# Performance work log

Measured on AMD Instinct MI355X. Metric: run time of the kernel, lower is better.

The kernel has to match this reference:

```python
import jax, jax.numpy as jnp
import numpy as np

H_DIM = 1024
GATE_DIM = 128


def setup_inputs() -> dict:
    key = jax.random.key(0)
    ks = jax.random.split(key, 7)
    B, L = 32, 2048
    bound_g = 1.0 / np.sqrt(GATE_DIM)
    bound_l = 1.0 / np.sqrt(GATE_DIM)
    return {
        "x": jax.random.normal(ks[0], (B, L, H_DIM), dtype=jnp.float32),
        # GRUCell params (PyTorch layout: rows ordered [r; z; n])
        "weight_ih": jax.random.uniform(ks[1], (3 * GATE_DIM, H_DIM), minval=-bound_g, maxval=bound_g, dtype=jnp.float32),
        "weight_hh": jax.random.uniform(ks[2], (3 * GATE_DIM, GATE_DIM), minval=-bound_g, maxval=bound_g, dtype=jnp.float32),
        "bias_ih": jax.random.uniform(ks[3], (3 * GATE_DIM,), minval=-bound_g, maxval=bound_g, dtype=jnp.float32),
        "bias_hh": jax.random.uniform(ks[4], (3 * GATE_DIM,), minval=-bound_g, maxval=bound_g, dtype=jnp.float32),
        # output linear (gate_dim -> 1)
        "lin_w": jax.random.uniform(ks[5], (1, GATE_DIM), minval=-bound_l, maxval=bound_l, dtype=jnp.float32),
        "lin_b": jax.random.uniform(ks[6], (1,), minval=-bound_l, maxval=bound_l, dtype=jnp.float32),
    }


def reference(x, weight_ih, weight_hh, bias_ih, bias_hh, lin_w, lin_b):
    """Faithful to the original PingHead.forward: `s` is never updated, so every
    timestep runs the GRUCell against a ZERO hidden state. weight_hh @ h == 0,
    leaving only bias_hh contributions. This lets us vectorize over (B, L)."""
    G = GATE_DIM
    # input projection for all gates: (B, L, 3G)
    gi = jnp.einsum('blh,gh->blg', x, weight_ih) + bias_ih
    i_r, i_z, i_n = gi[..., :G], gi[..., G:2 * G], gi[..., 2 * G:]
    b_hr, b_hz, b_hn = bias_hh[:G], bias_hh[G:2 * G], bias_hh[2 * G:]
    r = jax.nn.sigmoid(i_r + b_hr)
    z = jax.nn.sigmoid(i_z + b_hz)
    n = jnp.tanh(i_n + r * b_hn)
    h = (1.0 - z) * n  # + z * 0 (hidden state is always zero)
    # linear(gate_dim -> 1), squeeze last dim -> (B, L)
    out = jnp.einsum('blg,og->blo', h, lin_w) + lin_b
    return out[..., 0]
```

## Files before the change

### kernel.cpp

```cpp
#include <hip/hip_runtime.h>

#define H_DIM   1024
#define G_DIM   128
#define N_DIM   384
#define M_TOTAL 65536
#define BM      64
#define LDA     72

typedef _Float16 half8  __attribute__((ext_vector_type(8)));
typedef float    f32x4  __attribute__((ext_vector_type(4)));

__device__ __forceinline__ float sigmoidf_(float v) {
    return 1.0f / (1.0f + __expf(-v));
}

__global__ __launch_bounds__(256) void prep_w_kernel(const float* __restrict__ w,
                                                     _Float16* __restrict__ wf) {
    int gid  = blockIdx.x * 256 + threadIdx.x;
    int lane = gid & 63;
    int fid  = gid >> 6;
    int ktg  = fid & 31;
    int ct   = fid >> 5;
    int col  = ct * 16 + (lane & 15);
    int kb   = ktg * 32 + (lane >> 4) * 8;
    const f32x4* src = (const f32x4*)(w + (size_t)col * H_DIM + kb);
    f32x4 v0 = src[0], v1 = src[1];
    half8 h;
    #pragma unroll
    for (int j = 0; j < 4; ++j) { h[j] = (_Float16)v0[j]; h[4 + j] = (_Float16)v1[j]; }
    *(half8*)(wf + (size_t)gid * 8) = h;
}

__global__ __launch_bounds__(256) void ping_main_kernel(
    const float* __restrict__ x, const _Float16* __restrict__ wf,
    const float* __restrict__ bias_ih, const float* __restrict__ bias_hh,
    const float* __restrict__ lin_w, const float* __restrict__ lin_b,
    float* __restrict__ out)
{
    __shared__ _Float16 shA[BM * LDA];
    __shared__ float sh_out[BM];

    const int t    = threadIdx.x;
    const int lane = t & 63;
    const int wv   = t >> 6;
    const int ln   = lane & 15;
    const int quad = lane >> 4;

    if (t < BM) sh_out[t] = 0.0f;

    const size_t row0 = (size_t)blockIdx.x * BM;

    f32x4 acc[6][4];
    #pragma unroll
    for (int i = 0; i < 6; ++i)
        #pragma unroll
        for (int rt = 0; rt < 4; ++rt)
            acc[i][rt] = (f32x4){0.f, 0.f, 0.f, 0.f};

    const int rs = t >> 2;
    const int kg = (t & 3) * 16;
    const float* xrow = x + (row0 + rs) * (size_t)H_DIM + kg;
    _Float16* sA = &shA[rs * LDA + kg];

    const half8* bbase = (const half8*)wf;

    for (int kb = 0; kb < H_DIM / 64; ++kb) {
        __syncthreads();
        const f32x4* src = (const f32x4*)(xrow + kb * 64);
        f32x4 v0 = src[0], v1 = src[1], v2 = src[2], v3 = src[3];
        half8 h0, h1;
        #pragma unroll
        for (int j = 0; j < 4; ++j) {
            h0[j] = (_Float16)v0[j]; h0[4 + j] = (_Float16)v1[j];
            h1[j] = (_Float16)v2[j]; h1[4 + j] = (_Float16)v3[j];
        }
        *(half8*)sA       = h0;
        *(half8*)(sA + 8) = h1;
        __syncthreads();

        #pragma unroll
        for (int kt = 0; kt < 2; ++kt) {
            const int ktg = kb * 2 + kt;
            half8 a[4];
            #pragma unroll
            for (int rt = 0; rt < 4; ++rt)
                a[rt] = *(const half8*)&shA[(rt * 16 + ln) * LDA + kt * 32 + quad * 8];
            half8 b[6];
            #pragma unroll
            for (int i = 0; i < 6; ++i) {
                const int ct = ((i >> 1) * 8) + 2 * wv + (i & 1);
                b[i] = bbase[(size_t)(ct * 32 + ktg) * 64 + lane];
            }
            #pragma unroll
            for (int i = 0; i < 6; ++i)
                #pragma unroll
                for (int rt = 0; rt < 4; ++rt)
                    acc[i][rt] = __builtin_amdgcn_mfma_f32_16x16x32_f16(a[rt], b[i], acc[i][rt], 0, 0, 0);
        }
    }

    float psum[4][4];
    #pragma unroll
    for (int rt = 0; rt < 4; ++rt)
        #pragma unroll
        for (int reg = 0; reg < 4; ++reg)
            psum[rt][reg] = 0.f;

    #pragma unroll
    for (int i = 0; i < 2; ++i) {
        const int g = 32 * wv + 16 * i + ln;
        const float b_ir = bias_ih[g];
        const float b_iz = bias_ih[G_DIM + g];
        const float b_in = bias_ih[2 * G_DIM + g];
        const float b_hr = bias_hh[g];
        const float b_hz = bias_hh[G_DIM + g];
        const float b_hn = bias_hh[2 * G_DIM + g];
        const float lw   = lin_w[g];
        #pragma unroll
        for (int rt = 0; rt < 4; ++rt) {
            #pragma unroll
            for (int reg = 0; reg < 4; ++reg) {
                const float r = sigmoidf_(acc[i][rt][reg] + b_ir + b_hr);
                const float z = sigmoidf_(acc[2 + i][rt][reg] + b_iz + b_hz);
                const float n = tanhf(acc[4 + i][rt][reg] + b_in + r * b_hn);
                psum[rt][reg] += lw * (1.0f - z) * n;
            }
        }
    }

    #pragma unroll
    for (int rt = 0; rt < 4; ++rt)
        #pragma unroll
        for (int reg = 0; reg < 4; ++reg) {
            const int row = rt * 16 + quad * 4 + reg;
            atomicAdd(&sh_out[row], psum[rt][reg]);
        }

    __syncthreads();
    if (t < BM) out[row0 + t] = sh_out[t] + lin_b[0];
}

extern "C" void kernel_launch(void* const* d_in, const int* in_sizes, int n_in,
                              void* d_out, int out_size, void* d_ws, size_t ws_size,
                              hipStream_t stream) {
    const float* x      = (const float*)d_in[0];
    const float* w_ih   = (const float*)d_in[1];
    const float* b_ih   = (const float*)d_in[3];
    const float* b_hh   = (const float*)d_in[4];
    const float* lin_w  = (const float*)d_in[5];
    const float* lin_b  = (const float*)d_in[6];
    float* out          = (float*)d_out;
    _Float16* wf        = (_Float16*)d_ws;

    hipLaunchKernelGGL(prep_w_kernel, dim3((N_DIM / 16) * 32 * 64 / 256), dim3(256), 0, stream,
                       w_ih, wf);
    hipLaunchKernelGGL(ping_main_kernel, dim3(M_TOTAL / BM), dim3(256), 0, stream,
                       x, wf, b_ih, b_hh, lin_w, lin_b, out);
}
```

Measured before the change: 434.8 us.

## Double-buffer A tile in LDS with register prefetch, fast tanh and shuffle reduction

Adds a two-buffer LDS ring for the x tile. The next K-block's global loads are issued into registers before the MFMA work on the current block, so load latency is hidden and only one barrier per iteration remains. It also uses packed RTZ fp16 conversion, replaces tanhf with an exp-based formula, and reduces partial sums across lanes with xor shuffles before the LDS atomics. The costs are higher register and LDS use, plus slightly different rounding from round-toward-zero conversion.

```diff
diff --git a/kernel.cpp b/kernel.cpp
--- a/kernel.cpp
+++ b/kernel.cpp
@@ -6,12 +6,30 @@
 #define M_TOTAL 65536
 #define BM      64
 #define LDA     72
+#define ABUF    (BM * LDA)
 
 typedef _Float16 half8  __attribute__((ext_vector_type(8)));
+typedef __fp16   fp16x2 __attribute__((ext_vector_type(2)));
 typedef float    f32x4  __attribute__((ext_vector_type(4)));
 
-__device__ __forceinline__ float sigmoidf_(float v) {
+__device__ __forceinline__ float fast_sigmoid(float v) {
     return 1.0f / (1.0f + __expf(-v));
+}
+__device__ __forceinline__ float fast_tanh(float v) {
+    return 1.0f - 2.0f / (__expf(2.0f * v) + 1.0f);
+}
+
+__device__ __forceinline__ half8 cvt8(f32x4 a, f32x4 b) {
+    fp16x2 p0 = __builtin_amdgcn_cvt_pkrtz(a[0], a[1]);
+    fp16x2 p1 = __builtin_amdgcn_cvt_pkrtz(a[2], a[3]);
+    fp16x2 p2 = __builtin_amdgcn_cvt_pkrtz(b[0], b[1]);
+    fp16x2 p3 = __builtin_amdgcn_cvt_pkrtz(b[2], b[3]);
+    half8 h;
+    h[0] = (_Float16)p0[0]; h[1] = (_Float16)p0[1];
+    h[2] = (_Float16)p1[0]; h[3] = (_Float16)p1[1];
+    h[4] = (_Float16)p2[0]; h[5] = (_Float16)p2[1];
+    h[6] = (_Float16)p3[0]; h[7] = (_Float16)p3[1];
+    return h;
 }
 
 __global__ __launch_bounds__(256) void prep_w_kernel(const float* __restrict__ w,
@@ -37,7 +55,7 @@
     const float* __restrict__ lin_w, const float* __restrict__ lin_b,
     float* __restrict__ out)
 {
-    __shared__ _Float16 shA[BM * LDA];
+    __shared__ _Float16 shA[2 * ABUF];
     __shared__ float sh_out[BM];
 
     const int t    = threadIdx.x;
@@ -59,44 +77,54 @@
 
     const int rs = t >> 2;
     const int kg = (t & 3) * 16;
-    const float* xrow = x + (row0 + rs) * (size_t)H_DIM + kg;
-    _Float16* sA = &shA[rs * LDA + kg];
+    const float* xptr = x + (row0 + rs) * (size_t)H_DIM + kg;
+    _Float16* sW0 = &shA[rs * LDA + kg];
+    _Float16* sW1 = sW0 + ABUF;
 
-    const half8* bbase = (const half8*)wf;
+    const _Float16* pb[6];
+    #pragma unroll
+    for (int i = 0; i < 6; ++i) {
+        const int ct = ((i >> 1) * 8) + 2 * wv + (i & 1);
+        pb[i] = wf + ((size_t)(ct * 32) * 64 + lane) * 8;
+    }
 
-    for (int kb = 0; kb < H_DIM / 64; ++kb) {
-        __syncthreads();
-        const f32x4* src = (const f32x4*)(xrow + kb * 64);
-        f32x4 v0 = src[0], v1 = src[1], v2 = src[2], v3 = src[3];
-        half8 h0, h1;
-        #pragma unroll
-        for (int j = 0; j < 4; ++j) {
-            h0[j] = (_Float16)v0[j]; h0[4 + j] = (_Float16)v1[j];
-            h1[j] = (_Float16)v2[j]; h1[4 + j] = (_Float16)v3[j];
-        }
-        *(half8*)sA       = h0;
-        *(half8*)(sA + 8) = h1;
-        __syncthreads();
+    f32x4 q0, q1, q2, q3;
+    { const f32x4* s = (const f32x4*)xptr; q0 = s[0]; q1 = s[1]; q2 = s[2]; q3 = s[3]; xptr += 64; }
+    *(half8*)sW0       = cvt8(q0, q1);
+    *(half8*)(sW0 + 8) = cvt8(q2, q3);
+    __syncthreads();
 
+    #pragma unroll
+    for (int kb = 0; kb < 16; ++kb) {
+        const bool pref = (kb < 15);
+        if (pref) { const f32x4* s = (const f32x4*)xptr; q0 = s[0]; q1 = s[1]; q2 = s[2]; q3 = s[3]; xptr += 64; }
+
+        const _Float16* aRd = (kb & 1) ? (shA + ABUF) : shA;
         #pragma unroll
         for (int kt = 0; kt < 2; ++kt) {
-            const int ktg = kb * 2 + kt;
+            half8 b[6];
+            #pragma unroll
+            for (int i = 0; i < 6; ++i)
+                b[i] = *(const half8*)(pb[i] + kt * 512);
             half8 a[4];
             #pragma unroll
             for (int rt = 0; rt < 4; ++rt)
-                a[rt] = *(const half8*)&shA[(rt * 16 + ln) * LDA + kt * 32 + quad * 8];
-            half8 b[6];
-            #pragma unroll
-            for (int i = 0; i < 6; ++i) {
-                const int ct = ((i >> 1) * 8) + 2 * wv + (i & 1);
-                b[i] = bbase[(size_t)(ct * 32 + ktg) * 64 + lane];
-            }
+                a[rt] = *(const half8*)(aRd + (rt * 16 + ln) * LDA + kt * 32 + quad * 8);
             #pragma unroll
             for (int i = 0; i < 6; ++i)
                 #pragma unroll
                 for (int rt = 0; rt < 4; ++rt)
                     acc[i][rt] = __builtin_amdgcn_mfma_f32_16x16x32_f16(a[rt], b[i], acc[i][rt], 0, 0, 0);
         }
+        #pragma unroll
+        for (int i = 0; i < 6; ++i) pb[i] += 1024;
+
+        if (pref) {
+            _Float16* w = (kb & 1) ? sW0 : sW1;
+            *(half8*)w       = cvt8(q0, q1);
+            *(half8*)(w + 8) = cvt8(q2, q3);
+        }
+        __syncthreads();
     }
 
     float psum[4][4];
@@ -120,21 +148,26 @@
         for (int rt = 0; rt < 4; ++rt) {
             #pragma unroll
             for (int reg = 0; reg < 4; ++reg) {
-                const float r = sigmoidf_(acc[i][rt][reg] + b_ir + b_hr);
-                const float z = sigmoidf_(acc[2 + i][rt][reg] + b_iz + b_hz);
-                const float n = tanhf(acc[4 + i][rt][reg] + b_in + r * b_hn);
+                const float r = fast_sigmoid(acc[i][rt][reg] + b_ir + b_hr);
+                const float z = fast_sigmoid(acc[2 + i][rt][reg] + b_iz + b_hz);
+                const float n = fast_tanh(acc[4 + i][rt][reg] + b_in + r * b_hn);
                 psum[rt][reg] += lw * (1.0f - z) * n;
             }
         }
     }
 
     #pragma unroll
-    for (int rt = 0; rt < 4; ++rt)
+    for (int rt = 0; rt < 4; ++rt) {
         #pragma unroll
         for (int reg = 0; reg < 4; ++reg) {
-            const int row = rt * 16 + quad * 4 + reg;
-            atomicAdd(&sh_out[row], psum[rt][reg]);
+            float v = psum[rt][reg];
+            v += __shfl_xor(v, 1);
+            v += __shfl_xor(v, 2);
+            v += __shfl_xor(v, 4);
+            v += __shfl_xor(v, 8);
+            if (ln == 0) atomicAdd(&sh_out[rt * 16 + quad * 4 + reg], v);
         }
+    }
 
     __syncthreads();
     if (t < BM) out[row0 + t] = sh_out[t] + lin_b[0];
```

Result: slower. 469.7 us (+8.0%).
